# Performance work log

Hardware: AMD Instinct MI355X
Metric: run time of the kernel (lower is better)

## Reference

```python
import jax, jax.numpy as jnp
import numpy as np

HEADS = 16
DIM_HEAD = 64
RMS_EPS = 1e-12  # torch F.normalize default eps


def setup_inputs() -> dict:
    key = jax.random.key(0)
    k1, k2, k3 = jax.random.split(key, 3)
    b, n, dim = 2, 2048, 1024
    dim_inner = HEADS * DIM_HEAD
    x = jax.random.normal(k1, (b, n, dim), dtype=jnp.float32)
    gamma = jnp.ones((dim,), dtype=jnp.float32)
    w_qkv = jax.random.normal(k2, (dim, 3 * dim_inner), dtype=jnp.float32) * (dim ** -0.5)
    w_out = jax.random.normal(k3, (dim_inner, dim), dtype=jnp.float32) * (dim_inner ** -0.5)
    return {"x": x, "gamma": gamma, "w_qkv": w_qkv, "w_out": w_out}


def reference(x, gamma, w_qkv, w_out):
    b, n, dim = x.shape
    h, d = HEADS, DIM_HEAD
    # RMSNorm: F.normalize(x, dim=-1) * sqrt(dim) * gamma
    l2 = jnp.maximum(jnp.linalg.norm(x, axis=-1, keepdims=True), RMS_EPS)
    normed = x / l2 * (dim ** 0.5) * gamma
    # qkv projection, split order: (qkv h d)
    qkv = (normed @ w_qkv).reshape(b, n, 3, h, d)
    qkv = jnp.transpose(qkv, (2, 0, 3, 1, 4))  # [3, b, h, n, d]
    q, k, v = qkv[0], qkv[1], qkv[2]
    q = q * (d ** -0.5)
    sim = jnp.einsum('bhid,bhjd->bhij', q, k)  # [b,h,n,n]
    mask_value = -jnp.finfo(sim.dtype).max
    causal_mask = jnp.triu(jnp.ones((n, n), dtype=bool), k=1)
    sim = jnp.where(causal_mask, mask_value, sim)
    attn = jax.nn.softmax(sim, axis=-1)
    out = jnp.einsum('bhij,bhjd->bhid', attn, v)  # [b,h,n,d]
    out = jnp.transpose(out, (0, 2, 1, 3)).reshape(b, n, h * d)
    return out @ w_out
```

## Files before the change

### kernel.cpp

```cpp
#include <hip/hip_runtime.h>
#include <hip/hip_bf16.h>

#define BATCH 2
#define SEQ 2048
#define DMODEL 1024
#define NHEAD 16
#define DHEAD 64
#define NQKV 3072
#define DINNER 1024

typedef __attribute__((ext_vector_type(4))) short short4v;
typedef __attribute__((ext_vector_type(8))) short short8v;
typedef __attribute__((ext_vector_type(4))) float f32x4;

__device__ __forceinline__ unsigned short f2bf(float f) {
  union { float f; unsigned int u; } c; c.f = f;
  unsigned int u = c.u;
  u += 0x7fffu + ((u >> 16) & 1u);
  return (unsigned short)(u >> 16);
}

__device__ __forceinline__ float exp2_hw(float x) {
  float r;
  asm("v_exp_f32 %0, %1" : "=v"(r) : "v"(x));
  return r;
}

#define GL16(gp, lp)                                             \
  __builtin_amdgcn_global_load_lds(                              \
      (__attribute__((address_space(1))) void*)(gp),             \
      (__attribute__((address_space(3))) void*)(lp), 16, 0, 0)

#define FULL_BARRIER()                              \
  do {                                              \
    __builtin_amdgcn_sched_barrier(0);              \
    __builtin_amdgcn_s_barrier();                   \
    __builtin_amdgcn_sched_barrier(0);              \
  } while (0)

__global__ __launch_bounds__(256) void prep_kernel(const float* __restrict__ x,
                                                   const float* __restrict__ gamma,
                                                   const float* __restrict__ w_qkv,
                                                   const float* __restrict__ w_out,
                                                   unsigned short* __restrict__ normed,
                                                   unsigned short* __restrict__ wqkvT,
                                                   unsigned short* __restrict__ woutT) {
  __shared__ float tile[32][33];
  __shared__ float wss[4];
  const int b = blockIdx.x;
  const int t = threadIdx.x;
  if (b < 4096) {
    const float* in;
    unsigned short* out;
    int K, N, blk;
    if (b < 3072) { in = w_qkv; out = wqkvT; K = DMODEL; N = NQKV; blk = b; }
    else          { in = w_out; out = woutT; K = DINNER; N = DMODEL; blk = b - 3072; }
    const int tiles_n = N >> 5;
    const int tn = blk % tiles_n;
    const int tk = blk / tiles_n;
    const int k0 = tk << 5, n0 = tn << 5;
#pragma unroll
    for (int p = 0; p < 4; p++) {
      const int e = p * 256 + t;
      const int r = e >> 5, c = e & 31;
      tile[r][c] = in[(size_t)(k0 + r) * N + n0 + c];
    }
    __syncthreads();
#pragma unroll
    for (int p = 0; p < 4; p++) {
      const int e = p * 256 + t;
      const int r = e >> 5, c = e & 31;
      out[(size_t)(n0 + r) * K + k0 + c] = f2bf(tile[c][r]);
    }
  } else {
    const int row = b - 4096;
    const float* xr = x + (size_t)row * DMODEL;
    float4 v = ((const float4*)xr)[t];
    float ss = v.x * v.x + v.y * v.y + v.z * v.z + v.w * v.w;
#pragma unroll
    for (int off = 1; off < 64; off <<= 1) ss += __shfl_xor(ss, off);
    if ((t & 63) == 0) wss[t >> 6] = ss;
    __syncthreads();
    const float tot = wss[0] + wss[1] + wss[2] + wss[3];
    float l2 = sqrtf(tot);
    l2 = fmaxf(l2, 1e-12f);
    const float s = 32.0f / l2;
    const float4 gm = ((const float4*)gamma)[t];
    unsigned short o[4];
    o[0] = f2bf(v.x * s * gm.x);
    o[1] = f2bf(v.y * s * gm.y);
    o[2] = f2bf(v.z * s * gm.z);
    o[3] = f2bf(v.w * s * gm.w);
    unsigned short* op = normed + (size_t)row * DMODEL + t * 4;
    *(short4v*)op = *(short4v*)o;
  }
}

#define BM 128
#define BN 128
#define BKT 32
#define TILE_E (BM * BKT)
#define RNT (DMODEL / BKT)

__device__ void gemm_ring(const unsigned short* __restrict__ A,
                          const unsigned short* __restrict__ Bt, int rowBase,
                          int colBase, unsigned short (*sA)[TILE_E],
                          unsigned short (*sB)[TILE_E], f32x4 acc[4][4]) {
  const int t = threadIdx.x;
  const int lane = t & 63, wave = t >> 6;
  const int l15 = lane & 15, g = lane >> 4;
  const int wr = (wave >> 1) * 64, wc = (wave & 1) * 64;
#pragma unroll
  for (int m = 0; m < 4; m++)
#pragma unroll
    for (int n = 0; n < 4; n++) acc[m][n] = (f32x4){0.f, 0.f, 0.f, 0.f};
  const int r0 = t >> 2, j0 = t & 3;
  const int swz = (r0 >> 1) & 3;
  const unsigned short* Ag0 = A + (size_t)(rowBase + r0) * DMODEL + ((j0 ^ swz) * 8);
  const unsigned short* Ag1 = A + (size_t)(rowBase + r0 + 64) * DMODEL + ((j0 ^ swz) * 8);
  const unsigned short* Bg0 = Bt + (size_t)(colBase + r0) * DMODEL + ((j0 ^ swz) * 8);
  const unsigned short* Bg1 = Bt + (size_t)(colBase + r0 + 64) * DMODEL + ((j0 ^ swz) * 8);

#pragma unroll
  for (int tt = 0; tt < 2; ++tt) {
    GL16(Ag0 + tt * BKT, sA[tt] + t * 8);
    GL16(Ag1 + tt * BKT, sA[tt] + (t + 256) * 8);
    GL16(Bg0 + tt * BKT, sB[tt] + t * 8);
    GL16(Bg1 + tt * BKT, sB[tt] + (t + 256) * 8);
  }
  asm volatile("s_waitcnt vmcnt(4)" ::: "memory");
  FULL_BARRIER();

  for (int kt = 0; kt < RNT; ++kt) {
    const unsigned short* sAc = sA[kt % 3];
    const unsigned short* sBc = sB[kt % 3];
    const bool pf = (kt + 2 < RNT);
    if (pf) {
      const int nb = (kt + 2) % 3;
      const int ko = (kt + 2) * BKT;
      GL16(Ag0 + ko, sA[nb] + t * 8);
      GL16(Ag1 + ko, sA[nb] + (t + 256) * 8);
      GL16(Bg0 + ko, sB[nb] + t * 8);
      GL16(Bg1 + ko, sB[nb] + (t + 256) * 8);
    }
    short8v af[4], bf[4];
#pragma unroll
    for (int m = 0; m < 4; m++) {
      const int row = wr + m * 16 + l15;
      af[m] = *(const short8v*)(sAc + row * BKT + ((g ^ ((row >> 1) & 3)) * 8));
    }
#pragma unroll
    for (int n = 0; n < 4; n++) {
      const int row = wc + n * 16 + l15;
      bf[n] = *(const short8v*)(sBc + row * BKT + ((g ^ ((row >> 1) & 3)) * 8));
    }
    asm volatile("s_waitcnt lgkmcnt(0)" ::: "memory");
    __builtin_amdgcn_sched_barrier(0);
    __builtin_amdgcn_s_setprio(1);
#pragma unroll
    for (int m = 0; m < 4; m++)
#pragma unroll
      for (int n = 0; n < 4; n++)
        acc[m][n] = __builtin_amdgcn_mfma_f32_16x16x32_bf16(af[m], bf[n], acc[m][n], 0, 0, 0);
    __builtin_amdgcn_s_setprio(0);
    if (pf) asm volatile("s_waitcnt vmcnt(4)" ::: "memory");
    else    asm volatile("s_waitcnt vmcnt(0)" ::: "memory");
    FULL_BARRIER();
  }
}

__global__ __launch_bounds__(256, 3) void qkv_gemm_kernel(const unsigned short* __restrict__ A,
                                                          const unsigned short* __restrict__ Bt,
                                                          unsigned short* __restrict__ qb,
                                                          unsigned short* __restrict__ kb,
                                                          unsigned short* __restrict__ vtb) {
  __shared__ __align__(16) unsigned short sA[3][TILE_E];
  __shared__ __align__(16) unsigned short sB[3][TILE_E];
  const int nbn = NQKV / BN;
  const int bm = blockIdx.x / nbn, bn = blockIdx.x % nbn;
  f32x4 acc[4][4];
  gemm_ring(A, Bt, bm * BM, bn * BN, sA, sB, acc);
  const int t = threadIdx.x, lane = t & 63, wave = t >> 6;
  const int l15 = lane & 15, g = lane >> 4;
  const int wr = (wave >> 1) * 64, wc = (wave & 1) * 64;
#pragma unroll
  for (int m = 0; m < 4; m++)
#pragma unroll
    for (int n = 0; n < 4; n++) {
      const int col = bn * BN + wc + n * 16 + l15;
      const int part = col >> 10;
      const int h = (col >> 6) & 15;
      const int d = col & 63;
      const int row0 = bm * BM + wr + m * 16 + 4 * g;
      const int bb = row0 >> 11, i0 = row0 & 2047;
      if (part == 2) {
        const int ip = (i0 & ~31) | (((i0 >> 2) & 3) << 3) | (((i0 >> 4) & 1) << 2);
        union { short4v v; unsigned short u[4]; } pk;
#pragma unroll
        for (int r = 0; r < 4; r++) pk.u[r] = f2bf(acc[m][n][r]);
        *(short4v*)(vtb + ((size_t)(bb * NHEAD + h) * DHEAD + d) * SEQ + ip) = pk.v;
      } else {
#pragma unroll
        for (int r = 0; r < 4; r++) {
          const size_t idx = (((size_t)(bb * NHEAD + h)) * SEQ + i0 + r) * DHEAD + d;
          const float v = acc[m][n][r];
          if (part == 0) qb[idx] = f2bf(v * 0.18033688f);
          else kb[idx] = f2bf(v);
        }
      }
    }
}

__global__ __launch_bounds__(256, 3) void out_gemm_kernel(const unsigned short* __restrict__ A,
                                                          const unsigned short* __restrict__ Bt,
                                                          float* __restrict__ C) {
  __shared__ __align__(16) unsigned short sA[3][TILE_E];
  __shared__ __align__(16) unsigned short sB[3][TILE_E];
  const int nbn = DMODEL / BN;
  const int bm = blockIdx.x / nbn, bn = blockIdx.x % nbn;
  f32x4 acc[4][4];
  gemm_ring(A, Bt, bm * BM, bn * BN, sA, sB, acc);
  const int t = threadIdx.x, lane = t & 63, wave = t >> 6;
  const int l15 = lane & 15, g = lane >> 4;
  const int wr = (wave >> 1) * 64, wc = (wave & 1) * 64;
#pragma unroll
  for (int m = 0; m < 4; m++)
#pragma unroll
    for (int n = 0; n < 4; n++) {
      const int col = bn * BN + wc + n * 16 + l15;
#pragma unroll
      for (int r = 0; r < 4; r++) {
        const int row = bm * BM + wr + m * 16 + 4 * g + r;
        C[(size_t)row * DMODEL + col] = acc[m][n][r];
      }
    }
}

__global__ __launch_bounds__(256, 4) void attn_kernel(const unsigned short* __restrict__ qb,
                                                      const unsigned short* __restrict__ kb,
                                                      const unsigned short* __restrict__ vtb,
                                                      unsigned short* __restrict__ ob) {
  __shared__ __align__(16) unsigned short sK[2][64 * 64];
  __shared__ __align__(16) unsigned short sV[2][64 * 64];
  const int t = threadIdx.x, lane = t & 63, wave = t >> 6;
  const int l15 = lane & 15, g = lane >> 4;
  const int bh = blockIdx.x & 31;
  const int qord = blockIdx.x >> 5;
  const int qblk = (qord < 8) ? 31 - qord
                 : (qord < 16) ? qord - 8
                 : (qord < 24) ? 39 - qord
                 : qord - 16;
  const int qrow = qblk * 64 + wave * 16 + l15;
  const unsigned short* qptr = qb + (size_t)bh * SEQ * DHEAD;
  const unsigned short* kptr = kb + (size_t)bh * SEQ * DHEAD;
  const unsigned short* vtptr = vtb + (size_t)bh * DHEAD * SEQ;

  const int kr0 = t >> 3, kj0 = ((t & 7) ^ (kr0 & 7)) * 8;
  const int kr1 = kr0 + 32, kj1 = ((t & 7) ^ (kr1 & 7)) * 8;

  short8v qf[2];
#pragma unroll
  for (int kk = 0; kk < 2; kk++)
    qf[kk] = *(const short8v*)(qptr + (size_t)qrow * DHEAD + kk * 32 + 8 * g);

  union { short8v v; unsigned short u[8]; } ones;
#pragma unroll
  for (int j = 0; j < 8; j++) ones.u[j] = 0x3F80;

  float rm = -__builtin_inff();
  f32x4 acc_l = (f32x4){0.f, 0.f, 0.f, 0.f};
  f32x4 acc_o[4];
#pragma unroll
  for (int df = 0; df < 4; df++) acc_o[df] = (f32x4){0.f, 0.f, 0.f, 0.f};

  const int nsteps = qblk + 1;

  GL16(kptr + (size_t)kr0 * DHEAD + kj0, sK[0] + t * 8);
  GL16(kptr + (size_t)kr1 * DHEAD + kj1, sK[0] + (t + 256) * 8);
  GL16(vtptr + (size_t)kr0 * SEQ + kj0, sV[0] + t * 8);
  GL16(vtptr + (size_t)kr1 * SEQ + kj1, sV[0] + (t + 256) * 8);
  asm volatile("s_waitcnt vmcnt(0)" ::: "memory");
  FULL_BARRIER();

  int cur = 0;
  for (int s = 0; s < nsteps; ++s, cur ^= 1) {
    const int nxt = cur ^ 1;
    const bool more = (s + 1 < nsteps);
    if (more) {
      const int k0n = (s + 1) * 64;
      GL16(kptr + (size_t)(k0n + kr0) * DHEAD + kj0, sK[nxt] + t * 8);
      GL16(kptr + (size_t)(k0n + kr1) * DHEAD + kj1, sK[nxt] + (t + 256) * 8);
      GL16(vtptr + (size_t)kr0 * SEQ + k0n + kj0, sV[nxt] + t * 8);
      GL16(vtptr + (size_t)kr1 * SEQ + k0n + kj1, sV[nxt] + (t + 256) * 8);
    }
    {
      const int k0 = s * 64;
      const unsigned short* sKc = sK[cur];
      const unsigned short* sVc = sV[cur];
      short8v kf[4][2];
#pragma unroll
      for (int n4 = 0; n4 < 4; n4++) {
        const int row = n4 * 16 + l15;
#pragma unroll
        for (int kk = 0; kk < 2; kk++)
          kf[n4][kk] = *(const short8v*)(sKc + row * 64 + (((kk * 4 + g) ^ (row & 7)) * 8));
      }
      f32x4 s4[4];
#pragma unroll
      for (int n4 = 0; n4 < 4; n4++) s4[n4] = (f32x4){0.f, 0.f, 0.f, 0.f};
#pragma unroll
      for (int n4 = 0; n4 < 4; n4++)
#pragma unroll
        for (int kk = 0; kk < 2; kk++)
          s4[n4] = __builtin_amdgcn_mfma_f32_16x16x32_bf16(kf[n4][kk], qf[kk],
                                                           s4[n4], 0, 0, 0);
      if (s == nsteps - 1) {
#pragma unroll
        for (int n4 = 0; n4 < 4; n4++)
#pragma unroll
          for (int r = 0; r < 4; r++)
            if (k0 + n4 * 16 + 4 * g + r > qrow) s4[n4][r] = -__builtin_inff();
      }
      float mx = s4[0][0];
#pragma unroll
      for (int n4 = 0; n4 < 4; n4++)
#pragma unroll
        for (int r = 0; r < 4; r++)
          if (n4 || r) mx = fmaxf(mx, s4[n4][r]);
      if (!__all(mx <= rm)) {
        mx = fmaxf(mx, __shfl_xor(mx, 16));
        mx = fmaxf(mx, __shfl_xor(mx, 32));
        const float nm = fmaxf(rm, mx);
        const float al = exp2_hw(rm - nm);
        rm = nm;
#pragma unroll
        for (int r = 0; r < 4; r++) acc_l[r] *= al;
#pragma unroll
        for (int df = 0; df < 4; df++)
#pragma unroll
          for (int r = 0; r < 4; r++) acc_o[df][r] *= al;
      }
#pragma unroll
      for (int n4 = 0; n4 < 4; n4++)
#pragma unroll
        for (int r = 0; r < 4; r++) s4[n4][r] = exp2_hw(s4[n4][r] - rm);
      unsigned int pw[8];
#pragma unroll
      for (int n4 = 0; n4 < 4; n4++) {
        asm("v_cvt_pk_bf16_f32 %0, %1, %2"
            : "=v"(pw[n4 * 2]) : "v"(s4[n4][0]), "v"(s4[n4][1]));
        asm("v_cvt_pk_bf16_f32 %0, %1, %2"
            : "=v"(pw[n4 * 2 + 1]) : "v"(s4[n4][2]), "v"(s4[n4][3]));
      }
      union { short8v v; unsigned int wd[4]; } paA, paB;
      paA.wd[0] = pw[0]; paA.wd[1] = pw[1]; paA.wd[2] = pw[2]; paA.wd[3] = pw[3];
      paB.wd[0] = pw[4]; paB.wd[1] = pw[5]; paB.wd[2] = pw[6]; paB.wd[3] = pw[7];
      acc_l = __builtin_amdgcn_mfma_f32_16x16x32_bf16(ones.v, paA.v, acc_l, 0, 0, 0);
      acc_l = __builtin_amdgcn_mfma_f32_16x16x32_bf16(ones.v, paB.v, acc_l, 0, 0, 0);
#pragma unroll
      for (int df = 0; df < 4; df++) {
        const int row = df * 16 + l15;
        const short8v vfa = *(const short8v*)(sVc + row * 64 + (((g) ^ (row & 7)) * 8));
        acc_o[df] = __builtin_amdgcn_mfma_f32_16x16x32_bf16(vfa, paA.v, acc_o[df], 0, 0, 0);
        const short8v vfb = *(const short8v*)(sVc + row * 64 + (((4 + g) ^ (row & 7)) * 8));
        acc_o[df] = __builtin_amdgcn_mfma_f32_16x16x32_bf16(vfb, paB.v, acc_o[df], 0, 0, 0);
      }
    }
    if (more) {
      asm volatile("s_waitcnt vmcnt(0) lgkmcnt(0)" ::: "memory");
      FULL_BARRIER();
    }
  }

  const int bb = bh >> 4, hh = bh & 15;
  const float inv = 1.0f / acc_l[0];
#pragma unroll
  for (int df = 0; df < 4; df++) {
    union { short4v v; unsigned short u[4]; } pk4;
#pragma unroll
    for (int r = 0; r < 4; r++) pk4.u[r] = f2bf(acc_o[df][r] * inv);
    *(short4v*)(ob + ((size_t)bb * SEQ + qrow) * DINNER + hh * DHEAD + df * 16 + 4 * g) =
        pk4.v;
  }
}

extern "C" void kernel_launch(void* const* d_in, const int* in_sizes, int n_in,
                              void* d_out, int out_size, void* d_ws, size_t ws_size,
                              hipStream_t stream) {
  (void)in_sizes; (void)n_in; (void)out_size; (void)ws_size;
  const float* x = (const float*)d_in[0];
  const float* gamma = (const float*)d_in[1];
  const float* w_qkv = (const float*)d_in[2];
  const float* w_out = (const float*)d_in[3];
  float* out = (float*)d_out;
  char* ws = (char*)d_ws;
  unsigned short* wqkvT = (unsigned short*)(ws);
  unsigned short* woutT = (unsigned short*)(ws + 6291456);
  unsigned short* normed = (unsigned short*)(ws + 8388608);
  unsigned short* qbuf = (unsigned short*)(ws + 16777216);
  unsigned short* kbuf = (unsigned short*)(ws + 25165824);
  unsigned short* vtbuf = (unsigned short*)(ws + 33554432);
  unsigned short* aout = (unsigned short*)(ws + 41943040);

  hipLaunchKernelGGL(prep_kernel, dim3(8192), dim3(256), 0, stream,
                     x, gamma, w_qkv, w_out, normed, wqkvT, woutT);
  hipLaunchKernelGGL(qkv_gemm_kernel, dim3((BATCH * SEQ / BM) * (NQKV / BN)), dim3(256), 0,
                     stream, normed, wqkvT, qbuf, kbuf, vtbuf);
  hipLaunchKernelGGL(attn_kernel, dim3(BATCH * NHEAD * 32), dim3(256), 0, stream,
                     qbuf, kbuf, vtbuf, aout);
  hipLaunchKernelGGL(out_gemm_kernel, dim3((BATCH * SEQ / BM) * (DMODEL / BN)), dim3(256), 0,
                     stream, aout, woutT, out);
}
```

Baseline: 110.5 us.

## Split long causal attention rows into two KV halves with a combine kernel

```diff
diff --git a/kernel.cpp b/kernel.cpp
--- a/kernel.cpp
+++ b/kernel.cpp
@@ -18,6 +18,12 @@
   unsigned int u = c.u;
   u += 0x7fffu + ((u >> 16) & 1u);
   return (unsigned short)(u >> 16);
+}
+
+__device__ __forceinline__ float b2f(unsigned short u) {
+  union { unsigned int i; float f; } c;
+  c.i = ((unsigned int)u) << 16;
+  return c.f;
 }
 
 __device__ __forceinline__ float exp2_hw(float x) {
@@ -236,20 +242,33 @@
     }
 }
 
-__global__ __launch_bounds__(256, 4) void attn_kernel(const unsigned short* __restrict__ qb,
-                                                      const unsigned short* __restrict__ kb,
-                                                      const unsigned short* __restrict__ vtb,
-                                                      unsigned short* __restrict__ ob) {
+__global__ __launch_bounds__(256, 5) void attn_partial_kernel(
+    const unsigned short* __restrict__ qb, const unsigned short* __restrict__ kb,
+    const unsigned short* __restrict__ vtb, unsigned short* __restrict__ ob,
+    unsigned short* __restrict__ pO, float* __restrict__ pML) {
   __shared__ __align__(16) unsigned short sK[2][64 * 64];
   __shared__ __align__(16) unsigned short sV[2][64 * 64];
   const int t = threadIdx.x, lane = t & 63, wave = t >> 6;
   const int l15 = lane & 15, g = lane >> 4;
   const int bh = blockIdx.x & 31;
-  const int qord = blockIdx.x >> 5;
-  const int qblk = (qord < 8) ? 31 - qord
-                 : (qord < 16) ? qord - 8
-                 : (qord < 24) ? 39 - qord
-                 : qord - 16;
+  const int ord = blockIdx.x >> 5;
+  int qblk, s0, s1, half;
+  bool split;
+  if (ord < 32) {
+    const int j = 31 - ord;
+    qblk = 16 + (j >> 1);
+    half = j & 1;
+    const int nst = qblk + 1;
+    s0 = half ? (nst >> 1) : 0;
+    s1 = half ? nst : (nst >> 1);
+    split = true;
+  } else {
+    qblk = 47 - ord;
+    half = 0;
+    s0 = 0;
+    s1 = qblk + 1;
+    split = false;
+  }
   const int qrow = qblk * 64 + wave * 16 + l15;
   const unsigned short* qptr = qb + (size_t)bh * SEQ * DHEAD;
   const unsigned short* kptr = kb + (size_t)bh * SEQ * DHEAD;
@@ -273,19 +292,20 @@
 #pragma unroll
   for (int df = 0; df < 4; df++) acc_o[df] = (f32x4){0.f, 0.f, 0.f, 0.f};
 
-  const int nsteps = qblk + 1;
-
-  GL16(kptr + (size_t)kr0 * DHEAD + kj0, sK[0] + t * 8);
-  GL16(kptr + (size_t)kr1 * DHEAD + kj1, sK[0] + (t + 256) * 8);
-  GL16(vtptr + (size_t)kr0 * SEQ + kj0, sV[0] + t * 8);
-  GL16(vtptr + (size_t)kr1 * SEQ + kj1, sV[0] + (t + 256) * 8);
+  {
+    const int kb0 = s0 * 64;
+    GL16(kptr + (size_t)(kb0 + kr0) * DHEAD + kj0, sK[0] + t * 8);
+    GL16(kptr + (size_t)(kb0 + kr1) * DHEAD + kj1, sK[0] + (t + 256) * 8);
+    GL16(vtptr + (size_t)kr0 * SEQ + kb0 + kj0, sV[0] + t * 8);
+    GL16(vtptr + (size_t)kr1 * SEQ + kb0 + kj1, sV[0] + (t + 256) * 8);
+  }
   asm volatile("s_waitcnt vmcnt(0)" ::: "memory");
   FULL_BARRIER();
 
   int cur = 0;
-  for (int s = 0; s < nsteps; ++s, cur ^= 1) {
+  for (int s = s0; s < s1; ++s, cur ^= 1) {
     const int nxt = cur ^ 1;
-    const bool more = (s + 1 < nsteps);
+    const bool more = (s + 1 < s1);
     if (more) {
       const int k0n = (s + 1) * 64;
       GL16(kptr + (size_t)(k0n + kr0) * DHEAD + kj0, sK[nxt] + t * 8);
@@ -314,7 +334,7 @@
         for (int kk = 0; kk < 2; kk++)
           s4[n4] = __builtin_amdgcn_mfma_f32_16x16x32_bf16(kf[n4][kk], qf[kk],
                                                            s4[n4], 0, 0, 0);
-      if (s == nsteps - 1) {
+      if (s == qblk) {
 #pragma unroll
         for (int n4 = 0; n4 < 4; n4++)
 #pragma unroll
@@ -372,16 +392,70 @@
     }
   }
 
+  const float l = acc_l[0];
+  const float inv = 1.0f / l;
+  if (!split) {
+    const int bb = bh >> 4, hh = bh & 15;
+#pragma unroll
+    for (int df = 0; df < 4; df++) {
+      union { short4v v; unsigned short u[4]; } pk4;
+#pragma unroll
+      for (int r = 0; r < 4; r++) pk4.u[r] = f2bf(acc_o[df][r] * inv);
+      *(short4v*)(ob + ((size_t)bb * SEQ + qrow) * DINNER + hh * DHEAD + df * 16 + 4 * g) =
+          pk4.v;
+    }
+  } else {
+    const int chunk = (bh * 16 + (qblk - 16)) * 2 + half;
+    const int q = wave * 16 + l15;
+    unsigned short* po = pO + ((size_t)(chunk * 64 + q)) * 64;
+#pragma unroll
+    for (int df = 0; df < 4; df++) {
+      union { short4v v; unsigned short u[4]; } pk4;
+#pragma unroll
+      for (int r = 0; r < 4; r++) pk4.u[r] = f2bf(acc_o[df][r] * inv);
+      *(short4v*)(po + df * 16 + 4 * g) = pk4.v;
+    }
+    if (g == 0) {
+      float* ml = pML + (size_t)chunk * 128 + q * 2;
+      ml[0] = rm;
+      ml[1] = l;
+    }
+  }
+}
+
+__global__ __launch_bounds__(256) void attn_combine_kernel(
+    const unsigned short* __restrict__ pO, const float* __restrict__ pML,
+    unsigned short* __restrict__ ob) {
+  const int blk = blockIdx.x;
+  const int bh = blk & 31, qi = blk >> 5;
+  const int qblk = 16 + qi;
+  const int t = threadIdx.x;
+  const int q = t >> 2, ds = (t & 3) * 16;
+  const int chunk0 = (bh * 16 + qi) * 2;
+  const float m0 = pML[(size_t)chunk0 * 128 + q * 2];
+  const float l0 = pML[(size_t)chunk0 * 128 + q * 2 + 1];
+  const float m1 = pML[(size_t)(chunk0 + 1) * 128 + q * 2];
+  const float l1 = pML[(size_t)(chunk0 + 1) * 128 + q * 2 + 1];
+  const float M = fmaxf(m0, m1);
+  const float w0 = exp2_hw(m0 - M) * l0;
+  const float w1 = exp2_hw(m1 - M) * l1;
+  const float inv = 1.0f / (w0 + w1);
+  const unsigned short* o0 = pO + ((size_t)(chunk0 * 64 + q)) * 64 + ds;
+  const unsigned short* o1 = pO + ((size_t)((chunk0 + 1) * 64 + q)) * 64 + ds;
+  union { short8v v; unsigned short u[8]; } a0, a1, b0, b1, r0, r1;
+  a0.v = *(const short8v*)o0;
+  b0.v = *(const short8v*)(o0 + 8);
+  a1.v = *(const short8v*)o1;
+  b1.v = *(const short8v*)(o1 + 8);
+#pragma unroll
+  for (int j = 0; j < 8; j++) {
+    r0.u[j] = f2bf((w0 * b2f(a0.u[j]) + w1 * b2f(a1.u[j])) * inv);
+    r1.u[j] = f2bf((w0 * b2f(b0.u[j]) + w1 * b2f(b1.u[j])) * inv);
+  }
   const int bb = bh >> 4, hh = bh & 15;
-  const float inv = 1.0f / acc_l[0];
-#pragma unroll
-  for (int df = 0; df < 4; df++) {
-    union { short4v v; unsigned short u[4]; } pk4;
-#pragma unroll
-    for (int r = 0; r < 4; r++) pk4.u[r] = f2bf(acc_o[df][r] * inv);
-    *(short4v*)(ob + ((size_t)bb * SEQ + qrow) * DINNER + hh * DHEAD + df * 16 + 4 * g) =
-        pk4.v;
-  }
+  unsigned short* op = ob + ((size_t)bb * SEQ + qblk * 64 + q) * DINNER + hh * DHEAD + ds;
+  *(short8v*)op = r0.v;
+  *(short8v*)(op + 8) = r1.v;
 }
 
 extern "C" void kernel_launch(void* const* d_in, const int* in_sizes, int n_in,
@@ -401,13 +475,17 @@
   unsigned short* kbuf = (unsigned short*)(ws + 25165824);
   unsigned short* vtbuf = (unsigned short*)(ws + 33554432);
   unsigned short* aout = (unsigned short*)(ws + 41943040);
+  unsigned short* pO = normed;
+  float* pML = (float*)ws;
 
   hipLaunchKernelGGL(prep_kernel, dim3(8192), dim3(256), 0, stream,
                      x, gamma, w_qkv, w_out, normed, wqkvT, woutT);
   hipLaunchKernelGGL(qkv_gemm_kernel, dim3((BATCH * SEQ / BM) * (NQKV / BN)), dim3(256), 0,
                      stream, normed, wqkvT, qbuf, kbuf, vtbuf);
-  hipLaunchKernelGGL(attn_kernel, dim3(BATCH * NHEAD * 32), dim3(256), 0, stream,
-                     qbuf, kbuf, vtbuf, aout);
+  hipLaunchKernelGGL(attn_partial_kernel, dim3(BATCH * NHEAD * 48), dim3(256), 0, stream,
+                     qbuf, kbuf, vtbuf, aout, pO, pML);
+  hipLaunchKernelGGL(attn_combine_kernel, dim3(BATCH * NHEAD * 16), dim3(256), 0, stream,
+                     pO, pML, aout);
   hipLaunchKernelGGL(out_gemm_kernel, dim3((BATCH * SEQ / BM) * (DMODEL / BN)), dim3(256), 0,
                      stream, aout, woutT, out);
 }
```

New measurement: 118.2 us. 1.07x slower.
